# Kernel tuning notes

Hardware: AMD Instinct MI355X
Metric: run time of the kernel (lower is better)

Reference implementation:

```python
import jax, jax.numpy as jnp
import numpy as np

BN_EPS = 1e-5

def _pair_indices(f0, f1):
    row, col = [], []
    for i in range(f0):
        for j in range(i + 1, f1):
            row.append(i); col.append(j)
    return np.asarray(row, np.int32), np.asarray(col, np.int32)

def setup_inputs() -> dict:
    key = jax.random.key(0)
    ks = jax.random.split(key, 6)
    B, F0, F1, E = 4096, 32, 32, 32
    I = F0 * (F0 - 1) // 2  # 496 pairs for F0 == F1
    xi = jax.random.normal(ks[0], (B, F0, E), jnp.float32)
    xj = jax.random.normal(ks[1], (B, F1, E), jnp.float32)
    # xavier_uniform over (1, I, E): bound = sqrt(6/(I+E)) approximated by normal scale
    W = jax.random.normal(ks[2], (1, I, E), jnp.float32) * np.sqrt(2.0 / (I + E))
    bn_gamma = jnp.ones((I,), jnp.float32)
    bn_beta = jnp.zeros((I,), jnp.float32)
    attn_w = jax.random.normal(ks[3], (E, E), jnp.float32) / np.sqrt(E)
    attn_b = jnp.zeros((E,), jnp.float32)
    proj_w = jax.random.normal(ks[4], (E, 1), jnp.float32) / np.sqrt(E)
    proj_b = jnp.zeros((1,), jnp.float32)
    return {"xi": xi, "xj": xj, "W": W, "bn_gamma": bn_gamma, "bn_beta": bn_beta,
            "attn_w": attn_w, "attn_b": attn_b, "proj_w": proj_w, "proj_b": proj_b}

def reference(xi, xj, W, bn_gamma, bn_beta, attn_w, attn_b, proj_w, proj_b):
    f0, f1 = xi.shape[1], xj.shape[1]
    row, col = _pair_indices(f0, f1)
    p = xi[:, row, :]              # [B, I, E]
    q = xj[:, col, :]              # [B, I, E]
    out = p * q
    # BatchNorm1d(I) on [B, I, E] in training mode: stats over (batch, emb)
    mean = jnp.mean(out, axis=(0, 2), keepdims=True)
    var = jnp.mean(jnp.square(out - mean), axis=(0, 2), keepdims=True)
    out = (out - mean) * jax.lax.rsqrt(var + BN_EPS)
    out = out * bn_gamma[None, :, None] + bn_beta[None, :, None]
    out = out * W                   # broadcast [1, I, E]
    # attention: linear -> relu -> linear -> softmax over interaction dim
    h = jax.nn.relu(jnp.einsum('bie,ea->bia', out, attn_w) + attn_b)
    logits = jnp.einsum('bia,ao->bio', h, proj_w) + proj_b  # [B, I, 1]
    scores = jax.nn.softmax(logits, axis=1)
    return scores * out
```

## Files before the change

### kernel.cpp

```cpp
#include <hip/hip_runtime.h>

#define NB 4096
#define NF 32
#define NE 32
#define NI 496
#define BN_EPS 1e-5f
#define XPAD 36

#define SA_BLOCKS 512
#define SA_BPB    8
#define SA_CHUNK  4

typedef float f32x4_t __attribute__((ext_vector_type(4)));
typedef short bf16x8_t __attribute__((ext_vector_type(8)));

static __device__ __forceinline__ unsigned short f2bf(float f) {
    unsigned u = __builtin_bit_cast(unsigned, f);
    u = (u + 0x7FFFu + ((u >> 16) & 1u)) >> 16;
    return (unsigned short)u;
}

__device__ __forceinline__ void pair_rc_fast(int i, int& r, int& c) {
    int rr = (int)((63.0f - sqrtf(3969.0f - 8.0f * (float)i)) * 0.5f);
    int off = rr * (63 - rr) / 2;
    if (off > i) { --rr; off = rr * (63 - rr) / 2; }
    else {
        int off2 = (rr + 1) * (62 - rr) / 2;
        if (off2 <= i) { rr = rr + 1; off = off2; }
    }
    r = rr; c = rr + 1 + (i - off);
}

__global__ __launch_bounds__(256) void statsA(
        const float* __restrict__ xi, const float* __restrict__ xj,
        float* __restrict__ part) {
    __shared__ __attribute__((aligned(16))) float xi_l[SA_CHUNK * NF * XPAD];
    __shared__ __attribute__((aligned(16))) float xj_l[SA_CHUNK * NF * XPAD];
    const int t  = threadIdx.x;
    const int r  = t >> 3;
    const int cg = t & 7;

    float4 acc1[4] = {{0,0,0,0},{0,0,0,0},{0,0,0,0},{0,0,0,0}};
    float4 acc2[4] = {{0,0,0,0},{0,0,0,0},{0,0,0,0},{0,0,0,0}};

    for (int ch = 0; ch < SA_BPB / SA_CHUNK; ++ch) {
        const int b0 = blockIdx.x * SA_BPB + ch * SA_CHUNK;
        const float4* xs = (const float4*)(xi + (size_t)b0 * NF * NE);
        const float4* ys = (const float4*)(xj + (size_t)b0 * NF * NE);
        if (ch) __syncthreads();
        #pragma unroll
        for (int k = 0; k < 4; ++k) {
            const int idx = t + 256 * k;
            const int row = idx >> 3;
            const int e4  = idx & 7;
            *(float4*)&xi_l[row * XPAD + e4 * 4] = xs[idx];
            *(float4*)&xj_l[row * XPAD + e4 * 4] = ys[idx];
        }
        __syncthreads();
        #pragma unroll
        for (int bb = 0; bb < SA_CHUNK; ++bb) {
            const float* xr  = &xi_l[(bb * NF + r) * XPAD];
            const float* xc0 = &xj_l[(bb * NF) * XPAD];
            #pragma unroll
            for (int e4 = 0; e4 < 8; ++e4) {
                const float4 av = *(const float4*)&xr[e4 * 4];
                #pragma unroll
                for (int k = 0; k < 4; ++k) {
                    const int c = cg + 8 * k;
                    const float4 qv = *(const float4*)&xc0[c * XPAD + e4 * 4];
                    float px = av.x * qv.x, py = av.y * qv.y;
                    float pz = av.z * qv.z, pw = av.w * qv.w;
                    acc1[k].x += px; acc1[k].y += py;
                    acc1[k].z += pz; acc1[k].w += pw;
                    acc2[k].x += px * px; acc2[k].y += py * py;
                    acc2[k].z += pz * pz; acc2[k].w += pw * pw;
                }
            }
        }
    }

    float* dst = part + (size_t)blockIdx.x * 2048;
    #pragma unroll
    for (int k = 0; k < 4; ++k) {
        const int c = cg + 8 * k;
        const int j = r * 32 + c;
        float g1 = (acc1[k].x + acc1[k].y) + (acc1[k].z + acc1[k].w);
        float g2 = (acc2[k].x + acc2[k].y) + (acc2[k].z + acc2[k].w);
        *(float2*)&dst[2 * j] = make_float2(g1, g2);
    }
}

__global__ __launch_bounds__(256) void statsB(
        const float* __restrict__ part,
        const float* __restrict__ gamma, const float* __restrict__ beta,
        float* __restrict__ scale, float* __restrict__ shift) {
    __shared__ float red[256];
    const int t   = threadIdx.x;
    const int col = blockIdx.x * 64 + (t & 63);
    const int q   = t >> 6;
    float s = 0.f;
    #pragma unroll 8
    for (int p = q * 128; p < (q + 1) * 128; ++p)
        s += part[(size_t)p * 2048 + col];
    red[t] = s;
    __syncthreads();
    if (t < 64) red[t] = red[t] + red[t + 64] + red[t + 128] + red[t + 192];
    __syncthreads();
    if (t < 32) {
        const int cell = blockIdx.x * 32 + t;
        const int r = cell >> 5, c = cell & 31;
        if (c > r) {
            const float g1 = red[2 * t];
            const float g2 = red[2 * t + 1];
            const float invN = 1.0f / (float)(NB * NE);
            const float mean = g1 * invN;
            const float var  = g2 * invN - mean * mean;
            const int   i    = r * (63 - r) / 2 + (c - r - 1);
            const float sc   = gamma[i] / sqrtf(var + BN_EPS);
            scale[i] = sc;
            shift[i] = beta[i] - mean * sc;
        }
    }
}

__global__ __launch_bounds__(256) void main_kernel(
        const float* __restrict__ xi, const float* __restrict__ xj,
        const float* __restrict__ W,
        const float* __restrict__ attn_w, const float* __restrict__ attn_b,
        const float* __restrict__ proj_w, const float* __restrict__ proj_b,
        const float* __restrict__ scale, const float* __restrict__ shift,
        float* __restrict__ out) {
    __shared__ __attribute__((aligned(16))) float xi_l[NF * XPAD];
    __shared__ __attribute__((aligned(16))) float xj_l[NF * XPAD];
    __shared__ float ss_l[NI * 2];
    __shared__ float lg[NI];
    __shared__ int   rc_l[NI];
    __shared__ float redm[4], reds[4];

    const int b    = blockIdx.x;
    const int t    = threadIdx.x;
    const int lane = t & 63;
    const int wv   = t >> 6;

    {
        const float4* x4 = (const float4*)(xi + (size_t)b * NF * NE);
        const float4* y4 = (const float4*)(xj + (size_t)b * NF * NE);
        const int r  = t >> 3;
        const int e0 = (t & 7) * 4;
        *(float4*)&xi_l[r * XPAD + e0] = x4[t];
        *(float4*)&xj_l[r * XPAD + e0] = y4[t];
        for (int s = t; s < NI; s += 256) {
            ss_l[2*s]   = scale[s];
            ss_l[2*s+1] = shift[s];
            int rr, cc; pair_rc_fast(s, rr, cc);
            rc_l[s] = (rr << 5) | cc;
        }
    }

    bf16x8_t bfr0, bfr1;
    {
        const int n  = lane & 15;
        const int kc = (lane >> 4) * 8;
        #pragma unroll
        for (int j = 0; j < 8; ++j) {
            bfr0[j] = (short)f2bf(attn_w[(kc + j) * NE + n]);
            bfr1[j] = (short)f2bf(attn_w[(kc + j) * NE + n + 16]);
        }
    }
    const float abn0 = attn_b[lane & 15];
    const float abn1 = attn_b[(lane & 15) + 16];
    const float pwn0 = proj_w[lane & 15];
    const float pwn1 = proj_w[(lane & 15) + 16];
    const float pb   = proj_b[0];
    __syncthreads();

    for (int m = wv; m < 31; m += 4) {
        const int i  = m * 16 + (lane & 15);
        const int kc = (lane >> 4) * 8;
        const int rc = rc_l[i];
        const int r  = rc >> 5, c = rc & 31;
        const float sc = ss_l[2*i], sh = ss_l[2*i+1];
        const float4 a0 = *(const float4*)&xi_l[r * XPAD + kc];
        const float4 a1 = *(const float4*)&xi_l[r * XPAD + kc + 4];
        const float4 q0 = *(const float4*)&xj_l[c * XPAD + kc];
        const float4 q1 = *(const float4*)&xj_l[c * XPAD + kc + 4];
        const float4 w0 = *(const float4*)&W[i * NE + kc];
        const float4 w1 = *(const float4*)&W[i * NE + kc + 4];
        bf16x8_t af;
        af[0] = (short)f2bf(w0.x * (sc * a0.x * q0.x + sh));
        af[1] = (short)f2bf(w0.y * (sc * a0.y * q0.y + sh));
        af[2] = (short)f2bf(w0.z * (sc * a0.z * q0.z + sh));
        af[3] = (short)f2bf(w0.w * (sc * a0.w * q0.w + sh));
        af[4] = (short)f2bf(w1.x * (sc * a1.x * q1.x + sh));
        af[5] = (short)f2bf(w1.y * (sc * a1.y * q1.y + sh));
        af[6] = (short)f2bf(w1.z * (sc * a1.z * q1.z + sh));
        af[7] = (short)f2bf(w1.w * (sc * a1.w * q1.w + sh));

        f32x4_t c0 = {0.f, 0.f, 0.f, 0.f};
        f32x4_t c1 = {0.f, 0.f, 0.f, 0.f};
        c0 = __builtin_amdgcn_mfma_f32_16x16x32_bf16(af, bfr0, c0, 0, 0, 0);
        c1 = __builtin_amdgcn_mfma_f32_16x16x32_bf16(af, bfr1, c1, 0, 0, 0);
        #pragma unroll
        for (int j = 0; j < 4; ++j) {
            float v = fmaxf(c0[j] + abn0, 0.f) * pwn0
                    + fmaxf(c1[j] + abn1, 0.f) * pwn1;
            v += __shfl_xor(v, 1);
            v += __shfl_xor(v, 2);
            v += __shfl_xor(v, 4);
            v += __shfl_xor(v, 8);
            if ((lane & 15) == 0)
                lg[m * 16 + (lane >> 4) * 4 + j] = v + pb;
        }
    }
    __syncthreads();

    float m = -1e30f;
    for (int f = t; f < NI; f += 256) m = fmaxf(m, lg[f]);
    for (int off = 32; off; off >>= 1) m = fmaxf(m, __shfl_xor(m, off));
    if ((t & 63) == 0) redm[wv] = m;
    __syncthreads();
    m = fmaxf(fmaxf(redm[0], redm[1]), fmaxf(redm[2], redm[3]));

    float s = 0.f;
    for (int f = t; f < NI; f += 256) {
        const float e = expf(lg[f] - m);
        lg[f] = e;
        s += e;
    }
    for (int off = 32; off; off >>= 1) s += __shfl_xor(s, off);
    if ((t & 63) == 0) reds[wv] = s;
    __syncthreads();
    const float inv = 1.0f / ((reds[0] + reds[1]) + (reds[2] + reds[3]));

    for (int f = t; f < NI; f += 256) lg[f] *= inv;
    __syncthreads();

    const float4* W4 = (const float4*)W;
    float4* op4 = (float4*)(out + (size_t)b * NI * NE);
    for (int f4 = t; f4 < NI * 8; f4 += 256) {
        const int i  = f4 >> 3;
        const int e0 = (f4 & 7) * 4;
        const int rc = rc_l[i];
        const int r  = rc >> 5, c = rc & 31;
        const float sc = ss_l[2*i], sh = ss_l[2*i+1];
        const float score = lg[i];
        const float4 w = W4[f4];
        float4 res;
        res.x = score * (w.x * (sc * xi_l[r*XPAD+e0+0] * xj_l[c*XPAD+e0+0] + sh));
        res.y = score * (w.y * (sc * xi_l[r*XPAD+e0+1] * xj_l[c*XPAD+e0+1] + sh));
        res.z = score * (w.z * (sc * xi_l[r*XPAD+e0+2] * xj_l[c*XPAD+e0+2] + sh));
        res.w = score * (w.w * (sc * xi_l[r*XPAD+e0+3] * xj_l[c*XPAD+e0+3] + sh));
        op4[f4] = res;
    }
}

extern "C" void kernel_launch(void* const* d_in, const int* in_sizes, int n_in,
                              void* d_out, int out_size, void* d_ws, size_t ws_size,
                              hipStream_t stream) {
    const float* xi     = (const float*)d_in[0];
    const float* xj     = (const float*)d_in[1];
    const float* W      = (const float*)d_in[2];
    const float* gamma  = (const float*)d_in[3];
    const float* beta   = (const float*)d_in[4];
    const float* attn_w = (const float*)d_in[5];
    const float* attn_b = (const float*)d_in[6];
    const float* proj_w = (const float*)d_in[7];
    const float* proj_b = (const float*)d_in[8];
    float* out = (float*)d_out;

    float* part  = (float*)d_ws;
    float* scale = part + (size_t)SA_BLOCKS * 2048;
    float* shift = scale + 512;

    statsA<<<SA_BLOCKS, 256, 0, stream>>>(xi, xj, part);
    statsB<<<32, 256, 0, stream>>>(part, gamma, beta, scale, shift);
    main_kernel<<<NB, 256, 0, stream>>>(xi, xj, W, attn_w, attn_b,
                                        proj_w, proj_b, scale, shift, out);
}
```

Before: 122.4 us.

## Keep normalized interaction values in registers and reuse them for output

The normalized, W-scaled interaction values computed for the MFMA input are now kept in a 64-entry per-thread register array instead of being discarded. After the softmax, the output is written straight from these registers with the score folded in. This removes the second pass that recomputed the values from LDS and reloaded W, and it also drops one normalization loop and its barrier. The cost is higher register pressure, which the launch bound of 4 blocks per CU may turn into spills. The output store pattern also changes to two float4 writes per lane, covering 8 contiguous floats per lane.

```diff
diff --git a/kernel.cpp b/kernel.cpp
--- a/kernel.cpp
+++ b/kernel.cpp
@@ -123,7 +123,7 @@
     }
 }
 
-__global__ __launch_bounds__(256) void main_kernel(
+__global__ __launch_bounds__(256, 4) void main_kernel(
         const float* __restrict__ xi, const float* __restrict__ xj,
         const float* __restrict__ W,
         const float* __restrict__ attn_w, const float* __restrict__ attn_b,
@@ -141,6 +141,7 @@
     const int t    = threadIdx.x;
     const int lane = t & 63;
     const int wv   = t >> 6;
+    const int kc   = (lane >> 4) * 8;
 
     {
         const float4* x4 = (const float4*)(xi + (size_t)b * NF * NE);
@@ -159,8 +160,7 @@
 
     bf16x8_t bfr0, bfr1;
     {
-        const int n  = lane & 15;
-        const int kc = (lane >> 4) * 8;
+        const int n = lane & 15;
         #pragma unroll
         for (int j = 0; j < 8; ++j) {
             bfr0[j] = (short)f2bf(attn_w[(kc + j) * NE + n]);
@@ -174,42 +174,49 @@
     const float pb   = proj_b[0];
     __syncthreads();
 
-    for (int m = wv; m < 31; m += 4) {
-        const int i  = m * 16 + (lane & 15);
-        const int kc = (lane >> 4) * 8;
-        const int rc = rc_l[i];
-        const int r  = rc >> 5, c = rc & 31;
-        const float sc = ss_l[2*i], sh = ss_l[2*i+1];
-        const float4 a0 = *(const float4*)&xi_l[r * XPAD + kc];
-        const float4 a1 = *(const float4*)&xi_l[r * XPAD + kc + 4];
-        const float4 q0 = *(const float4*)&xj_l[c * XPAD + kc];
-        const float4 q1 = *(const float4*)&xj_l[c * XPAD + kc + 4];
-        const float4 w0 = *(const float4*)&W[i * NE + kc];
-        const float4 w1 = *(const float4*)&W[i * NE + kc + 4];
-        bf16x8_t af;
-        af[0] = (short)f2bf(w0.x * (sc * a0.x * q0.x + sh));
-        af[1] = (short)f2bf(w0.y * (sc * a0.y * q0.y + sh));
-        af[2] = (short)f2bf(w0.z * (sc * a0.z * q0.z + sh));
-        af[3] = (short)f2bf(w0.w * (sc * a0.w * q0.w + sh));
-        af[4] = (short)f2bf(w1.x * (sc * a1.x * q1.x + sh));
-        af[5] = (short)f2bf(w1.y * (sc * a1.y * q1.y + sh));
-        af[6] = (short)f2bf(w1.z * (sc * a1.z * q1.z + sh));
-        af[7] = (short)f2bf(w1.w * (sc * a1.w * q1.w + sh));
-
-        f32x4_t c0 = {0.f, 0.f, 0.f, 0.f};
-        f32x4_t c1 = {0.f, 0.f, 0.f, 0.f};
-        c0 = __builtin_amdgcn_mfma_f32_16x16x32_bf16(af, bfr0, c0, 0, 0, 0);
-        c1 = __builtin_amdgcn_mfma_f32_16x16x32_bf16(af, bfr1, c1, 0, 0, 0);
-        #pragma unroll
-        for (int j = 0; j < 4; ++j) {
-            float v = fmaxf(c0[j] + abn0, 0.f) * pwn0
-                    + fmaxf(c1[j] + abn1, 0.f) * pwn1;
-            v += __shfl_xor(v, 1);
-            v += __shfl_xor(v, 2);
-            v += __shfl_xor(v, 4);
-            v += __shfl_xor(v, 8);
-            if ((lane & 15) == 0)
-                lg[m * 16 + (lane >> 4) * 4 + j] = v + pb;
+    float o_reg[8][8];
+    #pragma unroll
+    for (int mt = 0; mt < 8; ++mt) {
+        const int m = wv + 4 * mt;
+        if (m < 31) {
+            const int i  = m * 16 + (lane & 15);
+            const int rc = rc_l[i];
+            const int r  = rc >> 5, c = rc & 31;
+            const float sc = ss_l[2*i], sh = ss_l[2*i+1];
+            const float4 a0 = *(const float4*)&xi_l[r * XPAD + kc];
+            const float4 a1 = *(const float4*)&xi_l[r * XPAD + kc + 4];
+            const float4 q0 = *(const float4*)&xj_l[c * XPAD + kc];
+            const float4 q1 = *(const float4*)&xj_l[c * XPAD + kc + 4];
+            const float4 w0 = *(const float4*)&W[i * NE + kc];
+            const float4 w1 = *(const float4*)&W[i * NE + kc + 4];
+            o_reg[mt][0] = w0.x * (sc * a0.x * q0.x + sh);
+            o_reg[mt][1] = w0.y * (sc * a0.y * q0.y + sh);
+            o_reg[mt][2] = w0.z * (sc * a0.z * q0.z + sh);
+            o_reg[mt][3] = w0.w * (sc * a0.w * q0.w + sh);
+            o_reg[mt][4] = w1.x * (sc * a1.x * q1.x + sh);
+            o_reg[mt][5] = w1.y * (sc * a1.y * q1.y + sh);
+            o_reg[mt][6] = w1.z * (sc * a1.z * q1.z + sh);
+            o_reg[mt][7] = w1.w * (sc * a1.w * q1.w + sh);
+
+            bf16x8_t af;
+            #pragma unroll
+            for (int j = 0; j < 8; ++j) af[j] = (short)f2bf(o_reg[mt][j]);
+
+            f32x4_t c0 = {0.f, 0.f, 0.f, 0.f};
+            f32x4_t c1 = {0.f, 0.f, 0.f, 0.f};
+            c0 = __builtin_amdgcn_mfma_f32_16x16x32_bf16(af, bfr0, c0, 0, 0, 0);
+            c1 = __builtin_amdgcn_mfma_f32_16x16x32_bf16(af, bfr1, c1, 0, 0, 0);
+            #pragma unroll
+            for (int j = 0; j < 4; ++j) {
+                float v = fmaxf(c0[j] + abn0, 0.f) * pwn0
+                        + fmaxf(c1[j] + abn1, 0.f) * pwn1;
+                v += __shfl_xor(v, 1);
+                v += __shfl_xor(v, 2);
+                v += __shfl_xor(v, 4);
+                v += __shfl_xor(v, 8);
+                if ((lane & 15) == 0)
+                    lg[m * 16 + (lane >> 4) * 4 + j] = v + pb;
+            }
         }
     }
     __syncthreads();
@@ -232,25 +239,26 @@
     __syncthreads();
     const float inv = 1.0f / ((reds[0] + reds[1]) + (reds[2] + reds[3]));
 
-    for (int f = t; f < NI; f += 256) lg[f] *= inv;
-    __syncthreads();
-
-    const float4* W4 = (const float4*)W;
-    float4* op4 = (float4*)(out + (size_t)b * NI * NE);
-    for (int f4 = t; f4 < NI * 8; f4 += 256) {
-        const int i  = f4 >> 3;
-        const int e0 = (f4 & 7) * 4;
-        const int rc = rc_l[i];
-        const int r  = rc >> 5, c = rc & 31;
-        const float sc = ss_l[2*i], sh = ss_l[2*i+1];
-        const float score = lg[i];
-        const float4 w = W4[f4];
-        float4 res;
-        res.x = score * (w.x * (sc * xi_l[r*XPAD+e0+0] * xj_l[c*XPAD+e0+0] + sh));
-        res.y = score * (w.y * (sc * xi_l[r*XPAD+e0+1] * xj_l[c*XPAD+e0+1] + sh));
-        res.z = score * (w.z * (sc * xi_l[r*XPAD+e0+2] * xj_l[c*XPAD+e0+2] + sh));
-        res.w = score * (w.w * (sc * xi_l[r*XPAD+e0+3] * xj_l[c*XPAD+e0+3] + sh));
-        op4[f4] = res;
+    float* outb = out + (size_t)b * NI * NE;
+    #pragma unroll
+    for (int mt = 0; mt < 8; ++mt) {
+        const int m2 = wv + 4 * mt;
+        if (m2 < 31) {
+            const int i = m2 * 16 + (lane & 15);
+            const float score = lg[i] * inv;
+            float4 r0, r1;
+            r0.x = o_reg[mt][0] * score;
+            r0.y = o_reg[mt][1] * score;
+            r0.z = o_reg[mt][2] * score;
+            r0.w = o_reg[mt][3] * score;
+            r1.x = o_reg[mt][4] * score;
+            r1.y = o_reg[mt][5] * score;
+            r1.z = o_reg[mt][6] * score;
+            r1.w = o_reg[mt][7] * score;
+            float* base = outb + i * NE + kc;
+            *(float4*)base       = r0;
+            *(float4*)(base + 4) = r1;
+        }
     }
 }
 
```

Result: no change. 123.7 us (+1.1%).

## Split main kernel into logits and output kernels; spread stats over more blocks

Applied to the files above, without the earlier changes.

The fused per-batch kernel becomes two kernels. One computes the attention logits and softmax scores and writes them to a workspace buffer. The other reloads the inputs and scores and writes the scaled output, which should lower per-kernel register and LDS pressure and raise occupancy. statsA now runs 2048 blocks of 2 batches each instead of 512 blocks of 8, adding parallelism, while statsB reads four times as many partials. The cost is an extra launch, rereading xi/xj and W, and a scores round trip through global memory.

```diff
diff --git a/kernel.cpp b/kernel.cpp
--- a/kernel.cpp
+++ b/kernel.cpp
@@ -7,9 +7,9 @@
 #define BN_EPS 1e-5f
 #define XPAD 36
 
-#define SA_BLOCKS 512
-#define SA_BPB    8
-#define SA_CHUNK  4
+#define SA_BLOCKS 2048
+#define SA_BPB    2
+#define SA_CHUNK  2
 
 typedef float f32x4_t __attribute__((ext_vector_type(4)));
 typedef short bf16x8_t __attribute__((ext_vector_type(8)));
@@ -43,38 +43,35 @@
     float4 acc1[4] = {{0,0,0,0},{0,0,0,0},{0,0,0,0},{0,0,0,0}};
     float4 acc2[4] = {{0,0,0,0},{0,0,0,0},{0,0,0,0},{0,0,0,0}};
 
-    for (int ch = 0; ch < SA_BPB / SA_CHUNK; ++ch) {
-        const int b0 = blockIdx.x * SA_BPB + ch * SA_CHUNK;
-        const float4* xs = (const float4*)(xi + (size_t)b0 * NF * NE);
-        const float4* ys = (const float4*)(xj + (size_t)b0 * NF * NE);
-        if (ch) __syncthreads();
+    const int b0 = blockIdx.x * SA_BPB;
+    const float4* xs = (const float4*)(xi + (size_t)b0 * NF * NE);
+    const float4* ys = (const float4*)(xj + (size_t)b0 * NF * NE);
+    #pragma unroll
+    for (int k = 0; k < SA_CHUNK * NF * 8 / 256; ++k) {
+        const int idx = t + 256 * k;
+        const int row = idx >> 3;
+        const int e4  = idx & 7;
+        *(float4*)&xi_l[row * XPAD + e4 * 4] = xs[idx];
+        *(float4*)&xj_l[row * XPAD + e4 * 4] = ys[idx];
+    }
+    __syncthreads();
+    #pragma unroll
+    for (int bb = 0; bb < SA_CHUNK; ++bb) {
+        const float* xr  = &xi_l[(bb * NF + r) * XPAD];
+        const float* xc0 = &xj_l[(bb * NF) * XPAD];
         #pragma unroll
-        for (int k = 0; k < 4; ++k) {
-            const int idx = t + 256 * k;
-            const int row = idx >> 3;
-            const int e4  = idx & 7;
-            *(float4*)&xi_l[row * XPAD + e4 * 4] = xs[idx];
-            *(float4*)&xj_l[row * XPAD + e4 * 4] = ys[idx];
-        }
-        __syncthreads();
-        #pragma unroll
-        for (int bb = 0; bb < SA_CHUNK; ++bb) {
-            const float* xr  = &xi_l[(bb * NF + r) * XPAD];
-            const float* xc0 = &xj_l[(bb * NF) * XPAD];
+        for (int e4 = 0; e4 < 8; ++e4) {
+            const float4 av = *(const float4*)&xr[e4 * 4];
             #pragma unroll
-            for (int e4 = 0; e4 < 8; ++e4) {
-                const float4 av = *(const float4*)&xr[e4 * 4];
-                #pragma unroll
-                for (int k = 0; k < 4; ++k) {
-                    const int c = cg + 8 * k;
-                    const float4 qv = *(const float4*)&xc0[c * XPAD + e4 * 4];
-                    float px = av.x * qv.x, py = av.y * qv.y;
-                    float pz = av.z * qv.z, pw = av.w * qv.w;
-                    acc1[k].x += px; acc1[k].y += py;
-                    acc1[k].z += pz; acc1[k].w += pw;
-                    acc2[k].x += px * px; acc2[k].y += py * py;
-                    acc2[k].z += pz * pz; acc2[k].w += pw * pw;
-                }
+            for (int k = 0; k < 4; ++k) {
+                const int c = cg + 8 * k;
+                const float4 qv = *(const float4*)&xc0[c * XPAD + e4 * 4];
+                float px = av.x * qv.x, py = av.y * qv.y;
+                float pz = av.z * qv.z, pw = av.w * qv.w;
+                acc1[k].x += px; acc1[k].y += py;
+                acc1[k].z += pz; acc1[k].w += pw;
+                acc2[k].x += px * px; acc2[k].y += py * py;
+                acc2[k].z += pz * pz; acc2[k].w += pw * pw;
             }
         }
     }
@@ -100,7 +97,7 @@
     const int q   = t >> 6;
     float s = 0.f;
     #pragma unroll 8
-    for (int p = q * 128; p < (q + 1) * 128; ++p)
+    for (int p = q * (SA_BLOCKS/4); p < (q + 1) * (SA_BLOCKS/4); ++p)
         s += part[(size_t)p * 2048 + col];
     red[t] = s;
     __syncthreads();
@@ -123,24 +120,24 @@
     }
 }
 
-__global__ __launch_bounds__(256) void main_kernel(
+__global__ __launch_bounds__(256) void logits_kernel(
         const float* __restrict__ xi, const float* __restrict__ xj,
         const float* __restrict__ W,
         const float* __restrict__ attn_w, const float* __restrict__ attn_b,
         const float* __restrict__ proj_w, const float* __restrict__ proj_b,
         const float* __restrict__ scale, const float* __restrict__ shift,
-        float* __restrict__ out) {
+        float* __restrict__ scores) {
     __shared__ __attribute__((aligned(16))) float xi_l[NF * XPAD];
     __shared__ __attribute__((aligned(16))) float xj_l[NF * XPAD];
     __shared__ float ss_l[NI * 2];
     __shared__ float lg[NI];
-    __shared__ int   rc_l[NI];
     __shared__ float redm[4], reds[4];
 
     const int b    = blockIdx.x;
     const int t    = threadIdx.x;
     const int lane = t & 63;
     const int wv   = t >> 6;
+    const int kc   = (lane >> 4) * 8;
 
     {
         const float4* x4 = (const float4*)(xi + (size_t)b * NF * NE);
@@ -152,15 +149,12 @@
         for (int s = t; s < NI; s += 256) {
             ss_l[2*s]   = scale[s];
             ss_l[2*s+1] = shift[s];
-            int rr, cc; pair_rc_fast(s, rr, cc);
-            rc_l[s] = (rr << 5) | cc;
         }
     }
 
     bf16x8_t bfr0, bfr1;
     {
-        const int n  = lane & 15;
-        const int kc = (lane >> 4) * 8;
+        const int n = lane & 15;
         #pragma unroll
         for (int j = 0; j < 8; ++j) {
             bfr0[j] = (short)f2bf(attn_w[(kc + j) * NE + n]);
@@ -176,9 +170,7 @@
 
     for (int m = wv; m < 31; m += 4) {
         const int i  = m * 16 + (lane & 15);
-        const int kc = (lane >> 4) * 8;
-        const int rc = rc_l[i];
-        const int r  = rc >> 5, c = rc & 31;
+        int r, c; pair_rc_fast(i, r, c);
         const float sc = ss_l[2*i], sh = ss_l[2*i+1];
         const float4 a0 = *(const float4*)&xi_l[r * XPAD + kc];
         const float4 a1 = *(const float4*)&xi_l[r * XPAD + kc + 4];
@@ -232,7 +224,41 @@
     __syncthreads();
     const float inv = 1.0f / ((reds[0] + reds[1]) + (reds[2] + reds[3]));
 
-    for (int f = t; f < NI; f += 256) lg[f] *= inv;
+    float* sb = scores + (size_t)b * NI;
+    for (int f = t; f < NI; f += 256) sb[f] = lg[f] * inv;
+}
+
+__global__ __launch_bounds__(256) void output_kernel(
+        const float* __restrict__ xi, const float* __restrict__ xj,
+        const float* __restrict__ W,
+        const float* __restrict__ scale, const float* __restrict__ shift,
+        const float* __restrict__ scores,
+        float* __restrict__ out) {
+    __shared__ __attribute__((aligned(16))) float xi_l[NF * XPAD];
+    __shared__ __attribute__((aligned(16))) float xj_l[NF * XPAD];
+    __shared__ float ss_l[NI * 2];
+    __shared__ float sc_l[NI];
+    __shared__ int   rc_l[NI];
+
+    const int b = blockIdx.x;
+    const int t = threadIdx.x;
+
+    {
+        const float4* x4 = (const float4*)(xi + (size_t)b * NF * NE);
+        const float4* y4 = (const float4*)(xj + (size_t)b * NF * NE);
+        const int r  = t >> 3;
+        const int e0 = (t & 7) * 4;
+        *(float4*)&xi_l[r * XPAD + e0] = x4[t];
+        *(float4*)&xj_l[r * XPAD + e0] = y4[t];
+        const float* sb = scores + (size_t)b * NI;
+        for (int s = t; s < NI; s += 256) {
+            ss_l[2*s]   = scale[s];
+            ss_l[2*s+1] = shift[s];
+            sc_l[s]     = sb[s];
+            int rr, cc; pair_rc_fast(s, rr, cc);
+            rc_l[s] = (rr << 5) | cc;
+        }
+    }
     __syncthreads();
 
     const float4* W4 = (const float4*)W;
@@ -243,7 +269,7 @@
         const int rc = rc_l[i];
         const int r  = rc >> 5, c = rc & 31;
         const float sc = ss_l[2*i], sh = ss_l[2*i+1];
-        const float score = lg[i];
+        const float score = sc_l[i];
         const float4 w = W4[f4];
         float4 res;
         res.x = score * (w.x * (sc * xi_l[r*XPAD+e0+0] * xj_l[c*XPAD+e0+0] + sh));
@@ -268,12 +294,14 @@
     const float* proj_b = (const float*)d_in[8];
     float* out = (float*)d_out;
 
-    float* part  = (float*)d_ws;
-    float* scale = part + (size_t)SA_BLOCKS * 2048;
-    float* shift = scale + 512;
+    float* part   = (float*)d_ws;
+    float* scale  = part + (size_t)SA_BLOCKS * 2048;
+    float* shift  = scale + 512;
+    float* scores = shift + 512;
 
     statsA<<<SA_BLOCKS, 256, 0, stream>>>(xi, xj, part);
     statsB<<<32, 256, 0, stream>>>(part, gamma, beta, scale, shift);
-    main_kernel<<<NB, 256, 0, stream>>>(xi, xj, W, attn_w, attn_b,
-                                        proj_w, proj_b, scale, shift, out);
-}
+    logits_kernel<<<NB, 256, 0, stream>>>(xi, xj, W, attn_w, attn_b,
+                                          proj_w, proj_b, scale, shift, scores);
+    output_kernel<<<NB, 256, 0, stream>>>(xi, xj, W, scale, shift, scores, out);
+}
```

After: 173.3 us. 41.6% more time.
